# Kernel optimization log

Hardware: AMD Instinct MI355X
Metric: run time of the kernel (lower is better)

## Reference

```python
import jax, jax.numpy as jnp
import numpy as np

N_HEADS = 16


def setup_inputs() -> dict:
    key = jax.random.key(0)
    k1, k2, k3 = jax.random.split(key, 3)
    d = 1024
    x = jax.random.normal(k1, (8, 1024, d), dtype=jnp.float32)
    w_qkv = jax.random.normal(k2, (d, 3 * d), dtype=jnp.float32) * (1.0 / np.sqrt(d))
    w_out = jax.random.normal(k3, (d, d), dtype=jnp.float32) * (1.0 / np.sqrt(d))
    b_out = jnp.zeros((d,), dtype=jnp.float32)
    return {"x": x, "w_qkv": w_qkv, "w_out": w_out, "b_out": b_out}


def reference(x, w_qkv, w_out, b_out):
    a, b, c = x.shape
    h = N_HEADS
    hd = c // h
    scale = 1.0 / (c ** 0.5)  # note: 1/sqrt(model_dim), not head_dim
    qkv = (x @ w_qkv).reshape(a, b, 3, h, hd)
    q, k, v = jnp.moveaxis(qkv, 2, 0)          # each (a, b, h, hd)
    q = jnp.swapaxes(q, 1, 2)                  # (a, h, b, hd)
    k = jnp.swapaxes(k, 1, 2)
    v = jnp.swapaxes(v, 1, 2)
    scores = jnp.einsum('ahqd,ahkd->ahqk', q, k) * scale  # (a, h, b, b)
    # Faithful to the source: softmax over dim=1 (the HEADS axis)
    attn = jax.nn.softmax(scores, axis=1)
    out = jnp.einsum('ahqk,ahkd->ahqd', attn, v)           # (a, h, b, hd)
    out = jnp.swapaxes(out, 1, 2).reshape(a, b, c)
    return out @ w_out + b_out
```

## Files before the change

kernel.cpp:

```cpp
#include <hip/hip_runtime.h>
#include <hip/hip_bf16.h>

typedef __attribute__((ext_vector_type(8))) short short8;
typedef __attribute__((ext_vector_type(4))) short short4e;
typedef __attribute__((ext_vector_type(4))) float f32x4;
typedef __attribute__((ext_vector_type(16))) float f32x16;
typedef __attribute__((ext_vector_type(4))) unsigned uint4v;

#define SC_LOG2E 0.04508422f
#define MFMA32(a, b, c) __builtin_amdgcn_mfma_f32_32x32x16_bf16(a, b, c, 0, 0, 0)

__device__ inline short bf16r(float f) {
    union { float f; unsigned u; } v; v.f = f;
    unsigned r = v.u + 0x7FFFu + ((v.u >> 16) & 1u);
    return (short)(r >> 16);
}
__device__ inline float bflo(unsigned u) {
    union { unsigned u; float f; } v; v.u = u << 16; return v.f;
}
__device__ inline float bfhi(unsigned u) {
    union { unsigned u; float f; } v; v.u = u & 0xffff0000u; return v.f;
}
#if __has_builtin(__builtin_amdgcn_exp2f)
__device__ inline float fexp2(float x) { return __builtin_amdgcn_exp2f(x); }
#else
__device__ inline float fexp2(float x) { return __expf(x * 0.6931471806f); }
#endif
__device__ inline unsigned cvt_pk_bf16(float lo, float hi) {
    unsigned r;
    asm("v_cvt_pk_bf16_f32 %0, %1, %2" : "=v"(r) : "v"(lo), "v"(hi));
    return r;
}
__device__ inline void perm32swap(unsigned& a, unsigned& b) {
    asm("v_permlane32_swap_b32 %0, %1" : "+v"(a), "+v"(b));
}

#define GLOAD_LDS16(gp, lp) __builtin_amdgcn_global_load_lds( \
    (const __attribute__((address_space(1))) unsigned int*)(gp), \
    (__attribute__((address_space(3))) unsigned int*)(lp), 16, 0, 0)

__global__ void castk(const float* __restrict__ in, short* __restrict__ out, int n4) {
    int i = blockIdx.x * 256 + threadIdx.x;
    if (i < n4) {
        float4 v = ((const float4*)in)[i];
        short4 o;
        o.x = bf16r(v.x); o.y = bf16r(v.y); o.z = bf16r(v.z); o.w = bf16r(v.w);
        ((short4*)out)[i] = o;
    }
}

__global__ void tcast(const float* __restrict__ src, short* __restrict__ dst, int R, int C,
                      int nscale, float sfac) {
    __shared__ float tile[32][33];
    int bi = blockIdx.x, bj = blockIdx.y;
    int tx = threadIdx.x & 31, ty = threadIdx.x >> 5;
#pragma unroll
    for (int p = 0; p < 4; p++)
        tile[ty + p * 8][tx] = src[(long)(bi * 32 + ty + p * 8) * C + bj * 32 + tx];
    __syncthreads();
#pragma unroll
    for (int p = 0; p < 4; p++) {
        int n = bj * 32 + ty + p * 8;
        float v = tile[tx][ty + p * 8];
        if (n < nscale) v *= sfac;
        dst[(long)n * R + bi * 32 + tx] = bf16r(v);
    }
}

template<int OUT_BF16>
__global__ __launch_bounds__(256, 3)
void gemm_bt(const short* __restrict__ A, const short* __restrict__ Bt,
             void* __restrict__ Cout, const float* __restrict__ bias,
             short* __restrict__ Vt,
             int M, int N, int K, int nbx, int cpx, int lda) {
    __shared__ short As[3][128 * 32];
    __shared__ short Bs[3][128 * 32];
    const int wg = blockIdx.x;
    const int lg = (wg & 7) * cpx + (wg >> 3);
    const int bx = lg % nbx, by = lg / nbx;
    const int tid = threadIdx.x, w = tid >> 6, lane = tid & 63;
    const int wr = w >> 1, wc = w & 1;
    const int l15 = lane & 15, lhi = lane >> 4;
    const int m0 = by * 128, n0 = bx * 128;
    f32x4 acc[4][4] = {};
    const int NT = K / 32;

    auto stage = [&](int buf, int t) {
        int k0 = t * 32;
#pragma unroll
        for (int j = 0; j < 2; j++) {
            int chunk = w * 128 + j * 64 + lane;
            int row = chunk >> 2, cp = chunk & 3;
            int cc = cp ^ ((row >> 1) & 3);
            GLOAD_LDS16(A  + (long)(m0 + row) * lda + k0 + cc * 8, &As[buf][chunk * 8]);
            GLOAD_LDS16(Bt + (long)(n0 + row) * K   + k0 + cc * 8, &Bs[buf][chunk * 8]);
        }
    };

    stage(0, 0);
    stage(1, 1);
    asm volatile("s_waitcnt vmcnt(4)\ns_barrier" ::: "memory");
    __builtin_amdgcn_sched_barrier(0);

    int bR = 0, bW = 2;
    for (int t = 0; t < NT; t++) {
        bool issued = (t + 2 < NT);
        if (issued) stage(bW, t + 2);
        const short* Ab = As[bR];
        const short* Bb = Bs[bR];
        short8 af[4], bfr[4];
#pragma unroll
        for (int i = 0; i < 4; i++) {
            int arow = wr * 64 + i * 16 + l15;
            int brow = wc * 64 + i * 16 + l15;
            af[i]  = *(const short8*)(Ab + arow * 32 + (lhi ^ ((arow >> 1) & 3)) * 8);
            bfr[i] = *(const short8*)(Bb + brow * 32 + (lhi ^ ((brow >> 1) & 3)) * 8);
        }
        __builtin_amdgcn_s_setprio(1);
#pragma unroll
        for (int i = 0; i < 4; i++)
#pragma unroll
            for (int j = 0; j < 4; j++)
                acc[i][j] = __builtin_amdgcn_mfma_f32_16x16x32_bf16(af[i], bfr[j], acc[i][j], 0, 0, 0);
        __builtin_amdgcn_s_setprio(0);
        if (issued) asm volatile("s_waitcnt vmcnt(4)\ns_barrier" ::: "memory");
        else        asm volatile("s_waitcnt vmcnt(0)\ns_barrier" ::: "memory");
        __builtin_amdgcn_sched_barrier(0);
        bR = (bR == 2) ? 0 : bR + 1;
        bW = (bW == 2) ? 0 : bW + 1;
    }
    if (OUT_BF16 && n0 >= 2048) {
        const int a = m0 >> 10, k0v = m0 & 1023;
#pragma unroll
        for (int i = 0; i < 4; i++)
#pragma unroll
            for (int j = 0; j < 4; j++) {
                int colp = n0 - 2048 + wc * 64 + j * 16 + l15;
                int k = k0v + wr * 64 + i * 16 + lhi * 4;
                short4e s4;
#pragma unroll
                for (int r = 0; r < 4; r++) s4[r] = bf16r(acc[i][j][r]);
                *(short4e*)(Vt + (long)a * 1048576 + (long)colp * 1024 + k) = s4;
            }
    } else {
#pragma unroll
        for (int i = 0; i < 4; i++)
#pragma unroll
            for (int j = 0; j < 4; j++)
#pragma unroll
                for (int r = 0; r < 4; r++) {
                    int row = m0 + wr * 64 + i * 16 + lhi * 4 + r;
                    int col = n0 + wc * 64 + j * 16 + l15;
                    float v = acc[i][j][r];
                    if (OUT_BF16) ((short*)Cout)[(long)row * N + col] = bf16r(v);
                    else          ((float*)Cout)[(long)row * N + col] = v + bias[col];
                }
    }
}

__global__ __launch_bounds__(256, 2)
void dsum_kernel(const short* __restrict__ qkv, unsigned* __restrict__ negL) {
    __shared__ short Qs[2][128 * 64];
    __shared__ short Ks[2][128 * 64];
    const int wg = blockIdx.x;
    const int lg = (wg & 7) * 64 + (wg >> 3);
    const int a = lg >> 6, q0 = ((lg >> 3) & 7) * 128, k0 = (lg & 7) * 128;
    const int tid = threadIdx.x, w = tid >> 6, lane = tid & 63;
    const int wr = w >> 1, wc = w & 1;
    const int l31 = lane & 31, hi = lane >> 5;
    const long qb = (long)a * 3145728;
    f32x16 dacc[2][2] = {};

    auto stage = [&](int buf, int hh) {
#pragma unroll
        for (int j = 0; j < 4; j++) {
            int c = j * 256 + tid;
            int row = c >> 3, cc = (c & 7) ^ (row & 7);
            GLOAD_LDS16(qkv + qb + (long)(q0 + row) * 3072 + hh * 64 + cc * 8,        &Qs[buf][c * 8]);
            GLOAD_LDS16(qkv + qb + (long)(k0 + row) * 3072 + 1024 + hh * 64 + cc * 8, &Ks[buf][c * 8]);
        }
    };

    stage(0, 0);
    __syncthreads();
    int buf = 0;
    for (int hh = 0; hh < 16; hh++) {
        if (hh < 15) stage(buf ^ 1, hh + 1);
        short8 ka[2][4], qf[2][4];
#pragma unroll
        for (int i = 0; i < 2; i++)
#pragma unroll
            for (int dc = 0; dc < 4; dc++) {
                int row = wr * 64 + i * 32 + l31;
                int ph = (dc * 2 + hi) ^ (row & 7);
                ka[i][dc] = *(const short8*)(&Ks[buf][row * 64 + ph * 8]);
            }
#pragma unroll
        for (int j = 0; j < 2; j++)
#pragma unroll
            for (int dc = 0; dc < 4; dc++) {
                int row = wc * 64 + j * 32 + l31;
                int ph = (dc * 2 + hi) ^ (row & 7);
                qf[j][dc] = *(const short8*)(&Qs[buf][row * 64 + ph * 8]);
            }
#pragma unroll
        for (int i = 0; i < 2; i++)
#pragma unroll
            for (int j = 0; j < 2; j++) {
                f32x16 s = {};
#pragma unroll
                for (int dc = 0; dc < 4; dc++)
                    s = MFMA32(ka[i][dc], qf[j][dc], s);
#pragma unroll
                for (int r = 0; r < 16; r++)
                    dacc[i][j][r] += fexp2(s[r]);
            }
        __syncthreads();
        buf ^= 1;
    }
#pragma unroll
    for (int i = 0; i < 2; i++)
#pragma unroll
        for (int j = 0; j < 2; j++) {
            int ktg = (k0 >> 5) + wr * 2 + i;
            int qtg = (q0 >> 5) + wc * 2 + j;
            unsigned pwv[8];
#pragma unroll
            for (int u = 0; u < 8; u++)
                pwv[u] = cvt_pk_bf16(-__log2f(dacc[i][j][2 * u]),
                                     -__log2f(dacc[i][j][2 * u + 1]));
            unsigned* dst = negL + (((long)(a * 32 + ktg) * 32 + qtg) << 9) + lane * 8;
            *(uint4v*)dst       = (uint4v){pwv[0], pwv[1], pwv[2], pwv[3]};
            *(uint4v*)(dst + 4) = (uint4v){pwv[4], pwv[5], pwv[6], pwv[7]};
        }
}

__global__ __launch_bounds__(256, 2)
void attn2_kernel(const short* __restrict__ qkv, const short* __restrict__ Vt,
                  const unsigned* __restrict__ negL, short* __restrict__ ctx) {
    __shared__ short lds[3 * 8192];
    const int wg = blockIdx.x;
    const int lg = (wg & 7) * 64 + (wg >> 3);
    const int a = lg >> 6, h = (lg >> 2) & 15, qblk = lg & 3;
    const int tid = threadIdx.x, w = tid >> 6, lane = tid & 63;
    const int l31 = lane & 31, hi = lane >> 5;
    const int qw = qblk * 256 + w * 64;
    const long qb = (long)a * 3145728;

    short8 qfrag[2][4];
#pragma unroll
    for (int qs = 0; qs < 2; qs++)
#pragma unroll
        for (int dc = 0; dc < 4; dc++)
            qfrag[qs][dc] = *(const short8*)(qkv + qb +
                (long)(qw + qs * 32 + l31) * 3072 + h * 64 + dc * 16 + hi * 8);

    const short* kcol  = qkv + qb + 1024 + h * 64;
    const short* vbase = Vt + (long)a * 1048576 + (long)(h * 64) * 1024;
    const unsigned* lbase = negL + (long)a * 524288 + (qw >> 5) * 512 + lane * 8;

    auto stage = [&](int buf, int t) {
        int k0 = t * 64;
#pragma unroll
        for (int j = 0; j < 2; j++) {
            GLOAD_LDS16(kcol + (long)(k0 + j * 32 + l31) * 3072 + w * 16 + hi * 8,
                        &lds[buf * 8192 + (j * 256 + tid) * 8]);
            int fidx = j * 4 + w, n = fidx >> 1, dt = fidx & 1;
            GLOAD_LDS16(vbase + (long)(dt * 32 + l31) * 1024 + k0 + n * 16 + hi * 8,
                        &lds[buf * 8192 + 4096 + (j * 256 + tid) * 8]);
        }
    };

    f32x16 oacc[2][2] = {};
    stage(0, 0);
    stage(1, 1);
    asm volatile("s_waitcnt vmcnt(4)\ns_barrier" ::: "memory");
    __builtin_amdgcn_sched_barrier(0);

    int bR = 0, bW = 2;
    for (int t = 0; t < 16; t++) {
        uint4v dm[2][2][2];
#pragma unroll
        for (int qs = 0; qs < 2; qs++)
#pragma unroll
            for (int kt = 0; kt < 2; kt++) {
                const unsigned* dp = lbase + (long)(t * 2 + kt) * 16384 + qs * 512;
                dm[qs][kt][0] = *(const uint4v*)dp;
                dm[qs][kt][1] = *(const uint4v*)(dp + 4);
            }
        if (t + 2 < 16) stage(bW, t + 2);

        const short* Kb = &lds[bR * 8192];
        const short* Vb = &lds[bR * 8192 + 4096];
#pragma unroll
        for (int kt = 0; kt < 2; kt++) {
            short8 ka[4];
#pragma unroll
            for (int dc = 0; dc < 4; dc++)
                ka[dc] = *(const short8*)(Kb + ((kt * 4 + dc) * 64 + lane) * 8);

            short8 pf[2][2];
#pragma unroll
            for (int qs = 0; qs < 2; qs++) {
                f32x16 s = {};
                __builtin_amdgcn_s_setprio(1);
#pragma unroll
                for (int dc = 0; dc < 4; dc++)
                    s = MFMA32(ka[dc], qfrag[qs][dc], s);
                __builtin_amdgcn_s_setprio(0);
                unsigned pw[8];
#pragma unroll
                for (int u = 0; u < 8; u++) {
                    unsigned d = dm[qs][kt][u >> 2][u & 3];
                    float e0 = fexp2(s[2 * u]     + bflo(d));
                    float e1 = fexp2(s[2 * u + 1] + bfhi(d));
                    pw[u] = cvt_pk_bf16(e0, e1);
                }
                perm32swap(pw[0], pw[2]); perm32swap(pw[1], pw[3]);
                perm32swap(pw[4], pw[6]); perm32swap(pw[5], pw[7]);
                union { uint4v u; short8 s8; } c0, c1;
                c0.u = (uint4v){pw[0], pw[1], pw[2], pw[3]};
                c1.u = (uint4v){pw[4], pw[5], pw[6], pw[7]};
                pf[qs][0] = c0.s8;
                pf[qs][1] = c1.s8;
            }
            __builtin_amdgcn_s_setprio(1);
#pragma unroll
            for (int dt = 0; dt < 2; dt++)
#pragma unroll
                for (int nn = 0; nn < 2; nn++) {
                    short8 vf = *(const short8*)(Vb + (((kt * 2 + nn) * 2 + dt) * 64 + lane) * 8);
#pragma unroll
                    for (int qs = 0; qs < 2; qs++)
                        oacc[qs][dt] = MFMA32(pf[qs][nn], vf, oacc[qs][dt]);
                }
            __builtin_amdgcn_s_setprio(0);
        }
        asm volatile("s_waitcnt vmcnt(4)\ns_barrier" ::: "memory");
        __builtin_amdgcn_sched_barrier(0);
        bR = (bR == 2) ? 0 : bR + 1;
        bW = (bW == 2) ? 0 : bW + 1;
    }
#pragma unroll
    for (int qs = 0; qs < 2; qs++)
#pragma unroll
        for (int dt = 0; dt < 2; dt++)
#pragma unroll
            for (int r = 0; r < 16; r++) {
                int q = qw + qs * 32 + (r & 3) + 8 * (r >> 2) + 4 * hi;
                int col = h * 64 + dt * 32 + l31;
                ctx[((long)a * 1024 + q) * 3072 + col] = bf16r(oacc[qs][dt][r]);
            }
}

extern "C" void kernel_launch(void* const* d_in, const int* in_sizes, int n_in,
                              void* d_out, int out_size, void* d_ws, size_t ws_size,
                              hipStream_t stream) {
    const float* x     = (const float*)d_in[0];
    const float* w_qkv = (const float*)d_in[1];
    const float* w_out = (const float*)d_in[2];
    const float* b_out = (const float*)d_in[3];
    float* out = (float*)d_out;

    char* ws = (char*)d_ws;
    short* wqkvT   = (short*)(ws);
    unsigned* negL = (unsigned*)(ws);
    short* xb    = (short*)(ws + 16777216);
    short* woT   = (short*)(ws + 33554432);
    short* qkv   = (short*)(ws + 35651584);
    short* Vt    = (short*)(ws + 85983232);
    short* ctx   = qkv + 2048;
    if (ws_size < 109051904u) return;

    castk<<<8192, 256, 0, stream>>>(x, xb, 2097152);
    tcast<<<dim3(32, 96), 256, 0, stream>>>(w_qkv, wqkvT, 1024, 3072, 1024, SC_LOG2E);
    tcast<<<dim3(32, 32), 256, 0, stream>>>(w_out, woT, 1024, 1024, 0, 1.0f);
    gemm_bt<1><<<1536, 256, 0, stream>>>(xb, wqkvT, (void*)qkv, nullptr, Vt, 8192, 3072, 1024, 24, 192, 1024);
    dsum_kernel<<<512, 256, 0, stream>>>(qkv, negL);
    attn2_kernel<<<512, 256, 0, stream>>>(qkv, Vt, negL, ctx);
    gemm_bt<0><<<512, 256, 0, stream>>>(ctx, woT, (void*)out, b_out, nullptr, 8192, 1024, 1024, 8, 64, 3072);
}
```

Before: 193.2 us.

## Replace QKV projection GEMM with 256x256-tile, 512-thread pipelined kernel

Adds a dedicated gemm256 kernel for the x·Wqkv projection. It uses 256x256 output tiles, 8 waves and a double-buffered 64-wide K pipeline with direct global-to-LDS loads and fine-grained waitcnt barriers. The larger tile raises arithmetic intensity and cuts the number of blocks from 1536 to 384, which reduces redundant A/B reloads. The cost is 128KB of LDS per block and heavy register use (32 accumulators per lane), which limits occupancy. Only 384 blocks across 256 CUs gives 1.5 waves, so tail imbalance is a risk.

```diff
diff --git a/kernel.cpp b/kernel.cpp
--- a/kernel.cpp
+++ b/kernel.cpp
@@ -39,6 +39,10 @@
     (const __attribute__((address_space(1))) unsigned int*)(gp), \
     (__attribute__((address_space(3))) unsigned int*)(lp), 16, 0, 0)
 
+#define WB10 do { asm volatile("s_waitcnt vmcnt(10)\ns_barrier" ::: "memory"); __builtin_amdgcn_sched_barrier(0); } while (0)
+#define WB4  do { asm volatile("s_waitcnt vmcnt(4)\ns_barrier"  ::: "memory"); __builtin_amdgcn_sched_barrier(0); } while (0)
+#define WB0  do { asm volatile("s_waitcnt vmcnt(0)\ns_barrier"  ::: "memory"); __builtin_amdgcn_sched_barrier(0); } while (0)
+
 __global__ void castk(const float* __restrict__ in, short* __restrict__ out, int n4) {
     int i = blockIdx.x * 256 + threadIdx.x;
     if (i < n4) {
@@ -67,11 +71,121 @@
     }
 }
 
+__global__ __launch_bounds__(512, 2)
+void gemm256(const short* __restrict__ A, const short* __restrict__ Bt,
+             short* __restrict__ qkv, short* __restrict__ Vt) {
+    __shared__ short lds[65536];
+    const int wg = blockIdx.x;
+    const int lg = (wg & 7) * 48 + (wg >> 3);
+    const int bx = lg % 12, by = lg / 12;
+    const int m0 = by * 256, n0 = bx * 256;
+    const int tid = threadIdx.x, w = tid >> 6, lane = tid & 63;
+    const int wm = w >> 2, wn = w & 3;
+    const int l15 = lane & 15, lhi = lane >> 4;
+    f32x4 acc[8][4] = {};
+
+    auto stA = [&](int t, int ks) {
+#pragma unroll
+        for (int j = 0; j < 2; j++) {
+            int c = j * 512 + tid;
+            int row = c >> 2, sl = c & 3;
+            GLOAD_LDS16(A + (long)(m0 + row) * 1024 + t * 64 + ks * 32 + ((sl ^ ((row >> 2) & 3)) * 8),
+                        &lds[((t & 1) * 2 + ks) * 8192 + c * 8]);
+        }
+    };
+    auto stB = [&](int t, int ks) {
+#pragma unroll
+        for (int j = 0; j < 2; j++) {
+            int c = j * 512 + tid;
+            int row = c >> 2, sl = c & 3;
+            GLOAD_LDS16(Bt + (long)(n0 + row) * 1024 + t * 64 + ks * 32 + ((sl ^ ((row >> 2) & 3)) * 8),
+                        &lds[32768 + ((t & 1) * 2 + ks) * 8192 + c * 8]);
+        }
+    };
+
+    short8 af[8], bf[2];
+    auto ldA = [&](int buf, int ks) {
+#pragma unroll
+        for (int fi = 0; fi < 8; fi++) {
+            int row = wm * 128 + fi * 16 + l15;
+            af[fi] = *(const short8*)(&lds[(buf * 2 + ks) * 8192 + row * 32 +
+                                           ((lhi ^ ((row >> 2) & 3)) * 8)]);
+        }
+    };
+    auto ldB = [&](int buf, int ks, int fh) {
+#pragma unroll
+        for (int u = 0; u < 2; u++) {
+            int row = wn * 64 + (fh * 2 + u) * 16 + l15;
+            bf[u] = *(const short8*)(&lds[32768 + (buf * 2 + ks) * 8192 + row * 32 +
+                                          ((lhi ^ ((row >> 2) & 3)) * 8)]);
+        }
+    };
+    auto mm = [&](int fh) {
+        __builtin_amdgcn_s_setprio(1);
+#pragma unroll
+        for (int fi = 0; fi < 8; fi++)
+#pragma unroll
+            for (int u = 0; u < 2; u++)
+                acc[fi][fh * 2 + u] = __builtin_amdgcn_mfma_f32_16x16x32_bf16(
+                    af[fi], bf[u], acc[fi][fh * 2 + u], 0, 0, 0);
+        __builtin_amdgcn_s_setprio(0);
+    };
+
+    stA(0, 0); stB(0, 0); stA(0, 1); stB(0, 1); stA(1, 0); stB(1, 0);
+
+    for (int i = 0; i < 8; i++) {
+        const int t0 = 2 * i;
+        stA(t0 + 1, 1); WB10;
+        ldA(0, 0); ldB(0, 0, 0); mm(0);
+        stB(t0 + 1, 1); WB10;
+        ldB(0, 0, 1); mm(1);
+        if (i < 7) stA(t0 + 2, 0);
+        WB10;
+        ldA(0, 1); ldB(0, 1, 0); mm(0);
+        if (i < 7) stB(t0 + 2, 0);
+        WB10;
+        ldB(0, 1, 1); mm(1);
+        if (i < 7) { stA(t0 + 2, 1); WB10; } else { WB4; }
+        ldA(1, 0); ldB(1, 0, 0); mm(0);
+        if (i < 7) { stB(t0 + 2, 1); WB10; } else { WB4; }
+        ldB(1, 0, 1); mm(1);
+        if (i < 7) { stA(t0 + 3, 0); WB10; } else { WB0; }
+        ldA(1, 1); ldB(1, 1, 0); mm(0);
+        if (i < 7) { stB(t0 + 3, 0); WB10; } else { WB0; }
+        ldB(1, 1, 1); mm(1);
+    }
+
+    if (n0 >= 2048) {
+        const int a = m0 >> 10, k0v = m0 & 1023;
+#pragma unroll
+        for (int fi = 0; fi < 8; fi++)
+#pragma unroll
+            for (int fj = 0; fj < 4; fj++) {
+                int colp = n0 - 2048 + wn * 64 + fj * 16 + l15;
+                int k = k0v + wm * 128 + fi * 16 + lhi * 4;
+                short4e s4;
+#pragma unroll
+                for (int r = 0; r < 4; r++) s4[r] = bf16r(acc[fi][fj][r]);
+                *(short4e*)(Vt + (long)a * 1048576 + (long)colp * 1024 + k) = s4;
+            }
+    } else {
+#pragma unroll
+        for (int fi = 0; fi < 8; fi++)
+#pragma unroll
+            for (int fj = 0; fj < 4; fj++)
+#pragma unroll
+                for (int r = 0; r < 4; r++) {
+                    int row = m0 + wm * 128 + fi * 16 + lhi * 4 + r;
+                    int col = n0 + wn * 64 + fj * 16 + l15;
+                    qkv[(long)row * 3072 + col] = bf16r(acc[fi][fj][r]);
+                }
+    }
+}
+
 template<int OUT_BF16>
 __global__ __launch_bounds__(256, 3)
 void gemm_bt(const short* __restrict__ A, const short* __restrict__ Bt,
              void* __restrict__ Cout, const float* __restrict__ bias,
-             short* __restrict__ Vt,
              int M, int N, int K, int nbx, int cpx, int lda) {
     __shared__ short As[3][128 * 32];
     __shared__ short Bs[3][128 * 32];
@@ -129,33 +243,18 @@
         bR = (bR == 2) ? 0 : bR + 1;
         bW = (bW == 2) ? 0 : bW + 1;
     }
-    if (OUT_BF16 && n0 >= 2048) {
-        const int a = m0 >> 10, k0v = m0 & 1023;
-#pragma unroll
-        for (int i = 0; i < 4; i++)
-#pragma unroll
-            for (int j = 0; j < 4; j++) {
-                int colp = n0 - 2048 + wc * 64 + j * 16 + l15;
-                int k = k0v + wr * 64 + i * 16 + lhi * 4;
-                short4e s4;
-#pragma unroll
-                for (int r = 0; r < 4; r++) s4[r] = bf16r(acc[i][j][r]);
-                *(short4e*)(Vt + (long)a * 1048576 + (long)colp * 1024 + k) = s4;
-            }
-    } else {
-#pragma unroll
-        for (int i = 0; i < 4; i++)
-#pragma unroll
-            for (int j = 0; j < 4; j++)
-#pragma unroll
-                for (int r = 0; r < 4; r++) {
-                    int row = m0 + wr * 64 + i * 16 + lhi * 4 + r;
-                    int col = n0 + wc * 64 + j * 16 + l15;
-                    float v = acc[i][j][r];
-                    if (OUT_BF16) ((short*)Cout)[(long)row * N + col] = bf16r(v);
-                    else          ((float*)Cout)[(long)row * N + col] = v + bias[col];
-                }
-    }
+#pragma unroll
+    for (int i = 0; i < 4; i++)
+#pragma unroll
+        for (int j = 0; j < 4; j++)
+#pragma unroll
+            for (int r = 0; r < 4; r++) {
+                int row = m0 + wr * 64 + i * 16 + lhi * 4 + r;
+                int col = n0 + wc * 64 + j * 16 + l15;
+                float v = acc[i][j][r];
+                if (OUT_BF16) ((short*)Cout)[(long)row * N + col] = bf16r(v);
+                else          ((float*)Cout)[(long)row * N + col] = v + bias[col];
+            }
 }
 
 __global__ __launch_bounds__(256, 2)
@@ -375,8 +474,8 @@
     castk<<<8192, 256, 0, stream>>>(x, xb, 2097152);
     tcast<<<dim3(32, 96), 256, 0, stream>>>(w_qkv, wqkvT, 1024, 3072, 1024, SC_LOG2E);
     tcast<<<dim3(32, 32), 256, 0, stream>>>(w_out, woT, 1024, 1024, 0, 1.0f);
-    gemm_bt<1><<<1536, 256, 0, stream>>>(xb, wqkvT, (void*)qkv, nullptr, Vt, 8192, 3072, 1024, 24, 192, 1024);
+    gemm256<<<384, 512, 0, stream>>>(xb, wqkvT, qkv, Vt);
     dsum_kernel<<<512, 256, 0, stream>>>(qkv, negL);
     attn2_kernel<<<512, 256, 0, stream>>>(qkv, Vt, negL, ctx);
-    gemm_bt<0><<<512, 256, 0, stream>>>(ctx, woT, (void*)out, b_out, nullptr, 8192, 1024, 1024, 8, 64, 3072);
-}
+    gemm_bt<0><<<512, 256, 0, stream>>>(ctx, woT, (void*)out, b_out, 8192, 1024, 1024, 8, 64, 3072);
+}
```

Result: no change. 193.4 us (+0.1%).
